# Performance work log

Hardware: AMD Instinct MI355X
Metric: run time of the kernel (lower is better)

The kernel has to match this reference:

```python
import jax, jax.numpy as jnp
import numpy as np

F = 256      # n_features
N = 128      # n_nodes
B = 4096     # batch


def setup_inputs() -> dict:
    key = jax.random.key(0)
    ks = jax.random.split(key, 11)
    s = lambda *sh: 1.0 / np.sqrt(sh[-2]) if len(sh) >= 2 else 1.0
    x = jax.random.normal(ks[0], (B, F), dtype=jnp.float32)
    # Block-diagonal weights: [F, in, out] per stage; biases [F, out]
    w1 = jax.random.normal(ks[1], (F, 1, N), dtype=jnp.float32)
    b1 = jax.random.normal(ks[2], (F, N), dtype=jnp.float32) * 0.01
    w2 = jax.random.normal(ks[3], (F, N, N), dtype=jnp.float32) / np.sqrt(N)
    b2 = jax.random.normal(ks[4], (F, N), dtype=jnp.float32) * 0.01
    w3 = jax.random.normal(ks[5], (F, N, N), dtype=jnp.float32) / np.sqrt(N)
    b3 = jax.random.normal(ks[6], (F, N), dtype=jnp.float32) * 0.01
    w4 = jax.random.normal(ks[7], (F, N, 1), dtype=jnp.float32) / np.sqrt(N)
    b4 = jax.random.normal(ks[8], (F, 1), dtype=jnp.float32) * 0.01
    # Final linear: [F, 1] weight, [1] bias
    lr_w = jax.random.normal(ks[9], (F, 1), dtype=jnp.float32) / np.sqrt(F)
    lr_b = jax.random.normal(ks[10], (1,), dtype=jnp.float32) * 0.01
    return {"x": x, "w1": w1, "b1": b1, "w2": w2, "b2": b2,
            "w3": w3, "b3": b3, "w4": w4, "b4": b4,
            "lr_w": lr_w, "lr_b": lr_b}


def reference(x, w1, b1, w2, b2, w3, b3, w4, b4, lr_w, lr_b):
    # Per-feature block-diagonal MLP chain with ReLU between stages.
    # x: [B, F] -> view each feature as a 1-dim input to its own subnet.
    h = x[:, :, None]                                   # [B, F, 1]
    h = jax.nn.relu(jnp.einsum('bfi,fio->bfo', h, w1) + b1)   # [B, F, N]
    h = jax.nn.relu(jnp.einsum('bfi,fio->bfo', h, w2) + b2)   # [B, F, N]
    h = jax.nn.relu(jnp.einsum('bfi,fio->bfo', h, w3) + b3)   # [B, F, N]
    h = jnp.einsum('bfi,fio->bfo', h, w4) + b4                # [B, F, 1]
    x_pre = h[:, :, 0]                                        # [B, F]
    return x_pre @ lr_w + lr_b                                # [B, 1]
```

## Files before the change

### kernel.cpp

```cpp
#include <hip/hip_runtime.h>
#include <hip/hip_bf16.h>

#define F_DIM 256
#define N_DIM 128
#define B_DIM 4096

typedef float f32x2v __attribute__((ext_vector_type(2)));
typedef float f32x4v __attribute__((ext_vector_type(4)));
typedef float f32x16v __attribute__((ext_vector_type(16)));
typedef short s16x8 __attribute__((ext_vector_type(8)));
typedef unsigned int u32x4v __attribute__((ext_vector_type(4)));

#define PIN(x) asm("" : "+v"(x))

__device__ __forceinline__ unsigned short f2bf(float f) {
  union { float f; unsigned u; } v; v.f = f;
  unsigned r = v.u + 0x7fffu + ((v.u >> 16) & 1u);
  return (unsigned short)(r >> 16);
}

__device__ __forceinline__ unsigned pk2(float a, float b) {
  union { __hip_bfloat16 h[2]; unsigned u; } v;
  v.h[0] = __float2bfloat16(a);
  v.h[1] = __float2bfloat16(b);
  return v.u;
}

__device__ __forceinline__ void gload16(const void* g, void* l) {
  __builtin_amdgcn_global_load_lds(
      (const __attribute__((address_space(1))) unsigned int*)g,
      (__attribute__((address_space(3))) unsigned int*)l, 16, 0, 0);
}

__device__ __forceinline__ s16x8 frag1(unsigned d) {
  u32x4v v = {d, 0u, 0u, 0u};
  return __builtin_bit_cast(s16x8, v);
}

struct frag2 { s16x8 lo, hi; };

__device__ __forceinline__ frag2 cvt2(f32x16v a) {
  unsigned P[8];
#pragma unroll
  for (int q = 0; q < 8; ++q) {
    unsigned pk = pk2(a[2 * q], a[2 * q + 1]);
    asm("v_pk_max_i16 %0, %1, 0" : "=v"(P[q]) : "v"(pk));
  }
  u32x4v lo = {P[0], P[1], P[2], P[3]};
  u32x4v hh = {P[4], P[5], P[6], P[7]};
  frag2 r;
  r.lo = __builtin_bit_cast(s16x8, lo);
  r.hi = __builtin_bit_cast(s16x8, hh);
  return r;
}

__global__ void prep_w(const float* __restrict__ w2, const float* __restrict__ w3,
                       unsigned int* __restrict__ wTs) {
  __shared__ float tile[128 * 130];
  int m = blockIdx.x;
  const float* src = (m < 256) ? (w2 + (size_t)m * 16384)
                               : (w3 + (size_t)(m - 256) * 16384);
  int t = threadIdx.x;
  for (int k = 0; k < 64; ++k) {
    int idx = k * 256 + t;
    int i = idx >> 7, o = idx & 127;
    tile[o * 130 + i] = src[idx];
  }
  __syncthreads();
  unsigned int* dst = wTs + (size_t)m * 8192;
  for (int k = 0; k < 32; ++k) {
    int idx = k * 256 + t;
    int o = idx >> 6, i2 = idx & 63;
    unsigned pk = (unsigned)f2bf(tile[o * 130 + 2 * i2]) |
                  ((unsigned)f2bf(tile[o * 130 + 2 * i2 + 1]) << 16);
    int w = i2 & 7;
    int i2p = (i2 & ~7) + ((w >> 1) & 1) * 4 + (w & 1) + (((w >> 2) & 1) << 1);
    dst[(o * 64) + (i2p ^ ((o & 15) << 2))] = pk;
  }
}

__global__ void prep_x(const float* __restrict__ x, float* __restrict__ xT) {
  __shared__ float tile[64][65];
  int btile = blockIdx.x & 63;
  int ftile = blockIdx.x >> 6;
  int t = threadIdx.x;
  for (int k = 0; k < 16; ++k) {
    int idx = k * 256 + t;
    int r = idx >> 6, c = idx & 63;
    tile[r][c] = x[(size_t)(btile * 64 + r) * F_DIM + ftile * 64 + c];
  }
  __syncthreads();
  for (int k = 0; k < 16; ++k) {
    int idx = k * 256 + t;
    int fr = idx >> 6, br = idx & 63;
    xT[(size_t)(ftile * 64 + fr) * B_DIM + btile * 64 + br] = tile[br][fr];
  }
}

__global__ __launch_bounds__(512, 2) void mlp_chain(
    const float* __restrict__ xT, const float* __restrict__ w1,
    const float* __restrict__ b1, const float* __restrict__ b2,
    const float* __restrict__ b3, const float* __restrict__ w4,
    const float* __restrict__ b4, const unsigned int* __restrict__ wTs,
    float* __restrict__ xp) {
  __shared__ __align__(16) char Wb[2][128 * 256];
  __shared__ __align__(16) float w4l[N_DIM];

  const int f    = blockIdx.x >> 1;
  const int half = blockIdx.x & 1;
  const int t    = threadIdx.x;
  const int lane = t & 63, wid = t >> 6;
  const int c32 = lane & 31, hi = lane >> 5;

  {
    const char* s2 = (const char*)(wTs + (size_t)f * 8192);
    const char* s3 = (const char*)(wTs + (size_t)(256 + f) * 8192);
#pragma unroll
    for (int c = 0; c < 4; ++c) {
      int off = (wid * 4 + c) * 1024;
      gload16(s2 + off + lane * 16, &Wb[0][off]);
    }
#pragma unroll
    for (int c = 0; c < 4; ++c) {
      int off = (wid * 4 + c) * 1024;
      gload16(s3 + off + lane * 16, &Wb[1][off]);
    }
    if (t < 32) *(f32x4v*)&w4l[t * 4] = *(const f32x4v*)&w4[f * N_DIM + t * 4];
  }

  unsigned a1d[4], a2d[4], a3d[4];
#pragma unroll
  for (int it = 0; it < 4; ++it) {
    int i = it * 32 + c32;
    float w1v = w1[f * N_DIM + i], b1v = b1[f * N_DIM + i];
    float b2v = b2[f * N_DIM + i], b3v = b3[f * N_DIM + i];
    a1d[it] = hi ? 0u : pk2(w1v, b1v);
    a2d[it] = hi ? 0u : pk2(0.f, b2v);
    a3d[it] = hi ? 0u : pk2(0.f, b3v);
  }
  const float b4f = b4[f];
  const float* xcol = xT + (size_t)f * B_DIM + half * 2048;
  float* xprow = xp + (size_t)f * B_DIM + half * 2048;

  const int wbase = c32 * 256 + (((lane & 15) ^ hi) << 4);
  int va[8];
#pragma unroll
  for (int m = 0; m < 8; ++m) { va[m] = wbase ^ (m << 5); PIN(va[m]); }
  const char* wb = &Wb[0][0];

  __syncthreads();

  const f32x16v zero = {0.f, 0.f, 0.f, 0.f, 0.f, 0.f, 0.f, 0.f,
                        0.f, 0.f, 0.f, 0.f, 0.f, 0.f, 0.f, 0.f};
  const f32x2v zz = {0.f, 0.f};

  float xvA = xcol[wid * 64 + c32];
  float xvB = xcol[wid * 64 + 32 + c32];
#pragma unroll 1
  for (int itb = 0; itb < 4; ++itb) {
    const int bb = itb * 512 + wid * 64;
    s16x8 BxA = frag1(hi ? 0u : pk2(xvA, 1.0f));
    s16x8 BxB = frag1(hi ? 0u : pk2(xvB, 1.0f));
    float xvA_n = (itb < 3) ? xcol[bb + 512 + c32] : 0.f;
    float xvB_n = (itb < 3) ? xcol[bb + 512 + 32 + c32] : 0.f;

    s16x8 h1A[8], h1B[8];
#pragma unroll
    for (int it = 0; it < 4; ++it) {
      f32x16v hA = __builtin_amdgcn_mfma_f32_32x32x16_bf16(frag1(a1d[it]), BxA,
                                                           zero, 0, 0, 0);
      frag2 rA = cvt2(hA);
      h1A[2 * it] = rA.lo;  h1A[2 * it + 1] = rA.hi;
      PIN(h1A[2 * it]);  PIN(h1A[2 * it + 1]);
      f32x16v hB = __builtin_amdgcn_mfma_f32_32x32x16_bf16(frag1(a1d[it]), BxB,
                                                           zero, 0, 0, 0);
      frag2 rB = cvt2(hB);
      h1B[2 * it] = rB.lo;  h1B[2 * it + 1] = rB.hi;
      PIN(h1B[2 * it]);  PIN(h1B[2 * it + 1]);
    }

    s16x8 h2A[8], h2B[8];
#pragma unroll
    for (int ntp = 0; ntp < 2; ++ntp) {
      const int nt0 = 2 * ntp, nt1 = nt0 + 1;
      f32x16v bi0 = __builtin_amdgcn_mfma_f32_32x32x16_bf16(frag1(a2d[nt0]), BxA,
                                                            zero, 0, 0, 0);
      f32x16v bi1 = __builtin_amdgcn_mfma_f32_32x32x16_bf16(frag1(a2d[nt1]), BxA,
                                                            zero, 0, 0, 0);
      f32x16v u0A, u0B, u1A, u1B;
      __builtin_amdgcn_s_setprio(1);
#pragma unroll
      for (int m = 0; m < 8; ++m) {
        s16x8 af0 = *(const s16x8*)(wb + va[m] + nt0 * 8192);
        s16x8 af1 = *(const s16x8*)(wb + va[m] + nt1 * 8192);
        u0A = __builtin_amdgcn_mfma_f32_32x32x16_bf16(af0, h1A[m],
                                                      m == 0 ? bi0 : u0A, 0, 0, 0);
        u0B = __builtin_amdgcn_mfma_f32_32x32x16_bf16(af0, h1B[m],
                                                      m == 0 ? bi0 : u0B, 0, 0, 0);
        u1A = __builtin_amdgcn_mfma_f32_32x32x16_bf16(af1, h1A[m],
                                                      m == 0 ? bi1 : u1A, 0, 0, 0);
        u1B = __builtin_amdgcn_mfma_f32_32x32x16_bf16(af1, h1B[m],
                                                      m == 0 ? bi1 : u1B, 0, 0, 0);
      }
      __builtin_amdgcn_s_setprio(0);
      frag2 r0A = cvt2(u0A);
      h2A[2 * nt0] = r0A.lo;  h2A[2 * nt0 + 1] = r0A.hi;
      PIN(h2A[2 * nt0]);  PIN(h2A[2 * nt0 + 1]);
      frag2 r0B = cvt2(u0B);
      h2B[2 * nt0] = r0B.lo;  h2B[2 * nt0 + 1] = r0B.hi;
      PIN(h2B[2 * nt0]);  PIN(h2B[2 * nt0 + 1]);
      frag2 r1A = cvt2(u1A);
      h2A[2 * nt1] = r1A.lo;  h2A[2 * nt1 + 1] = r1A.hi;
      PIN(h2A[2 * nt1]);  PIN(h2A[2 * nt1 + 1]);
      frag2 r1B = cvt2(u1B);
      h2B[2 * nt1] = r1B.lo;  h2B[2 * nt1 + 1] = r1B.hi;
      PIN(h2B[2 * nt1]);  PIN(h2B[2 * nt1 + 1]);
    }

    f32x2v pA0 = zz, pA1 = zz, pB0 = zz, pB1 = zz;
#pragma unroll
    for (int n3p = 0; n3p < 2; ++n3p) {
      const int n30 = 2 * n3p, n31 = n30 + 1;
      f32x16v ci0 = __builtin_amdgcn_mfma_f32_32x32x16_bf16(frag1(a3d[n30]), BxA,
                                                            zero, 0, 0, 0);
      f32x16v ci1 = __builtin_amdgcn_mfma_f32_32x32x16_bf16(frag1(a3d[n31]), BxA,
                                                            zero, 0, 0, 0);
      f32x16v v0A, v0B, v1A, v1B;
      __builtin_amdgcn_s_setprio(1);
#pragma unroll
      for (int k = 0; k < 8; ++k) {
        s16x8 af0 = *(const s16x8*)(wb + va[k] + 32768 + n30 * 8192);
        s16x8 af1 = *(const s16x8*)(wb + va[k] + 32768 + n31 * 8192);
        v0A = __builtin_amdgcn_mfma_f32_32x32x16_bf16(af0, h2A[k],
                                                      k == 0 ? ci0 : v0A, 0, 0, 0);
        v0B = __builtin_amdgcn_mfma_f32_32x32x16_bf16(af0, h2B[k],
                                                      k == 0 ? ci0 : v0B, 0, 0, 0);
        v1A = __builtin_amdgcn_mfma_f32_32x32x16_bf16(af1, h2A[k],
                                                      k == 0 ? ci1 : v1A, 0, 0, 0);
        v1B = __builtin_amdgcn_mfma_f32_32x32x16_bf16(af1, h2B[k],
                                                      k == 0 ? ci1 : v1B, 0, 0, 0);
      }
      __builtin_amdgcn_s_setprio(0);
#pragma unroll
      for (int q = 0; q < 4; ++q) {
        f32x2v w01_0 = *(const f32x2v*)&w4l[n30 * 32 + q * 8 + hi * 4];
        f32x2v w23_0 = *(const f32x2v*)&w4l[n30 * 32 + q * 8 + hi * 4 + 2];
        f32x2v w01_1 = *(const f32x2v*)&w4l[n31 * 32 + q * 8 + hi * 4];
        f32x2v w23_1 = *(const f32x2v*)&w4l[n31 * 32 + q * 8 + hi * 4 + 2];
        f32x2v r;
        r[0] = fmaxf(v0A[4 * q + 0], 0.f); r[1] = fmaxf(v0A[4 * q + 1], 0.f);
        pA0 += r * w01_0;
        r[0] = fmaxf(v0A[4 * q + 2], 0.f); r[1] = fmaxf(v0A[4 * q + 3], 0.f);
        pA1 += r * w23_0;
        r[0] = fmaxf(v1A[4 * q + 0], 0.f); r[1] = fmaxf(v1A[4 * q + 1], 0.f);
        pA0 += r * w01_1;
        r[0] = fmaxf(v1A[4 * q + 2], 0.f); r[1] = fmaxf(v1A[4 * q + 3], 0.f);
        pA1 += r * w23_1;
        r[0] = fmaxf(v0B[4 * q + 0], 0.f); r[1] = fmaxf(v0B[4 * q + 1], 0.f);
        pB0 += r * w01_0;
        r[0] = fmaxf(v0B[4 * q + 2], 0.f); r[1] = fmaxf(v0B[4 * q + 3], 0.f);
        pB1 += r * w23_0;
        r[0] = fmaxf(v1B[4 * q + 0], 0.f); r[1] = fmaxf(v1B[4 * q + 1], 0.f);
        pB0 += r * w01_1;
        r[0] = fmaxf(v1B[4 * q + 2], 0.f); r[1] = fmaxf(v1B[4 * q + 3], 0.f);
        pB1 += r * w23_1;
      }
    }
    float pA = pA0[0] + pA0[1] + pA1[0] + pA1[1];
    float pB = pB0[0] + pB0[1] + pB1[0] + pB1[1];
    pA += __shfl_xor(pA, 32, 64);
    pB += __shfl_xor(pB, 32, 64);
    if (hi == 0) {
      xprow[bb + c32]      = pA + b4f;
      xprow[bb + 32 + c32] = pB + b4f;
    }
    xvA = xvA_n;
    xvB = xvB_n;
  }
}

__global__ void final_reduce(const float* __restrict__ xp,
                             const float* __restrict__ lr_w,
                             const float* __restrict__ lr_b,
                             float* __restrict__ out) {
  __shared__ float lw[F_DIM];
  __shared__ float part[4][64];
  int t = threadIdx.x;
  if (t < F_DIM) lw[t] = lr_w[t];
  __syncthreads();
  int q = t >> 6, bl = t & 63;
  int b = blockIdx.x * 64 + bl;
  float acc = 0.f;
#pragma unroll 8
  for (int j = 0; j < 64; ++j) {
    int ff = q * 64 + j;
    acc += xp[(size_t)ff * B_DIM + b] * lw[ff];
  }
  part[q][bl] = acc;
  __syncthreads();
  if (q == 0)
    out[b] = part[0][bl] + part[1][bl] + part[2][bl] + part[3][bl] + lr_b[0];
}

extern "C" void kernel_launch(void* const* d_in, const int* in_sizes, int n_in,
                              void* d_out, int out_size, void* d_ws, size_t ws_size,
                              hipStream_t stream) {
  (void)in_sizes; (void)n_in; (void)out_size; (void)ws_size;
  const float* x    = (const float*)d_in[0];
  const float* w1   = (const float*)d_in[1];
  const float* b1   = (const float*)d_in[2];
  const float* w2   = (const float*)d_in[3];
  const float* b2   = (const float*)d_in[4];
  const float* w3   = (const float*)d_in[5];
  const float* b3   = (const float*)d_in[6];
  const float* w4   = (const float*)d_in[7];
  const float* b4   = (const float*)d_in[8];
  const float* lr_w = (const float*)d_in[9];
  const float* lr_b = (const float*)d_in[10];
  float* out = (float*)d_out;

  char* ws = (char*)d_ws;
  unsigned int* wTs = (unsigned int*)ws;
  float* xT = (float*)(ws + (16u << 20));
  float* xp = (float*)(ws + (16u << 20) + (4u << 20));

  prep_w<<<512, 256, 0, stream>>>(w2, w3, wTs);
  prep_x<<<256, 256, 0, stream>>>(x, xT);
  mlp_chain<<<512, 512, 0, stream>>>(xT, w1, b1, b2, b3, w4, b4, wTs, xp);
  final_reduce<<<64, 256, 0, stream>>>(xp, lr_w, lr_b, out);
}
```

Measured before the change: 92.73 us.

## Split each feature across four smaller blocks and prefetch LDS weight fragments

The MLP kernel now launches 1024 blocks of 256 threads, four per feature, in place of 512 blocks of 512 threads. This gives finer scheduling granularity but makes each block reload the full 64KB of w2/w3 weights into LDS. The stage-2 and stage-3 inner loops now load the first four weight fragments into registers before the bias MFMAs and fetch the second half while the first-half MFMAs run, to hide LDS latency. The extra fragment arrays raise register pressure, and the weight staging traffic from global memory doubles.

```diff
diff --git a/kernel.cpp b/kernel.cpp
--- a/kernel.cpp
+++ b/kernel.cpp
@@ -97,7 +97,7 @@
   }
 }
 
-__global__ __launch_bounds__(512, 2) void mlp_chain(
+__global__ __launch_bounds__(256, 2) void mlp_chain(
     const float* __restrict__ xT, const float* __restrict__ w1,
     const float* __restrict__ b1, const float* __restrict__ b2,
     const float* __restrict__ b3, const float* __restrict__ w4,
@@ -106,9 +106,9 @@
   __shared__ __align__(16) char Wb[2][128 * 256];
   __shared__ __align__(16) float w4l[N_DIM];
 
-  const int f    = blockIdx.x >> 1;
-  const int half = blockIdx.x & 1;
-  const int t    = threadIdx.x;
+  const int f  = blockIdx.x >> 2;
+  const int qt = blockIdx.x & 3;
+  const int t  = threadIdx.x;
   const int lane = t & 63, wid = t >> 6;
   const int c32 = lane & 31, hi = lane >> 5;
 
@@ -116,13 +116,13 @@
     const char* s2 = (const char*)(wTs + (size_t)f * 8192);
     const char* s3 = (const char*)(wTs + (size_t)(256 + f) * 8192);
 #pragma unroll
-    for (int c = 0; c < 4; ++c) {
-      int off = (wid * 4 + c) * 1024;
+    for (int c = 0; c < 8; ++c) {
+      int off = (wid * 8 + c) * 1024;
       gload16(s2 + off + lane * 16, &Wb[0][off]);
     }
 #pragma unroll
-    for (int c = 0; c < 4; ++c) {
-      int off = (wid * 4 + c) * 1024;
+    for (int c = 0; c < 8; ++c) {
+      int off = (wid * 8 + c) * 1024;
       gload16(s3 + off + lane * 16, &Wb[1][off]);
     }
     if (t < 32) *(f32x4v*)&w4l[t * 4] = *(const f32x4v*)&w4[f * N_DIM + t * 4];
@@ -139,8 +139,8 @@
     a3d[it] = hi ? 0u : pk2(0.f, b3v);
   }
   const float b4f = b4[f];
-  const float* xcol = xT + (size_t)f * B_DIM + half * 2048;
-  float* xprow = xp + (size_t)f * B_DIM + half * 2048;
+  const float* xcol = xT + (size_t)f * B_DIM + qt * 1024;
+  float* xprow = xp + (size_t)f * B_DIM + qt * 1024;
 
   const int wbase = c32 * 256 + (((lane & 15) ^ hi) << 4);
   int va[8];
@@ -158,11 +158,11 @@
   float xvB = xcol[wid * 64 + 32 + c32];
 #pragma unroll 1
   for (int itb = 0; itb < 4; ++itb) {
-    const int bb = itb * 512 + wid * 64;
+    const int bb = itb * 256 + wid * 64;
     s16x8 BxA = frag1(hi ? 0u : pk2(xvA, 1.0f));
     s16x8 BxB = frag1(hi ? 0u : pk2(xvB, 1.0f));
-    float xvA_n = (itb < 3) ? xcol[bb + 512 + c32] : 0.f;
-    float xvB_n = (itb < 3) ? xcol[bb + 512 + 32 + c32] : 0.f;
+    float xvA_n = (itb < 3) ? xcol[bb + 256 + c32] : 0.f;
+    float xvB_n = (itb < 3) ? xcol[bb + 256 + 32 + c32] : 0.f;
 
     s16x8 h1A[8], h1B[8];
 #pragma unroll
@@ -183,24 +183,40 @@
 #pragma unroll
     for (int ntp = 0; ntp < 2; ++ntp) {
       const int nt0 = 2 * ntp, nt1 = nt0 + 1;
+      s16x8 p0[4], p1[4];
+#pragma unroll
+      for (int j = 0; j < 4; ++j) {
+        p0[j] = *(const s16x8*)(wb + va[j] + nt0 * 8192);
+        p1[j] = *(const s16x8*)(wb + va[j] + nt1 * 8192);
+        PIN(p0[j]); PIN(p1[j]);
+      }
       f32x16v bi0 = __builtin_amdgcn_mfma_f32_32x32x16_bf16(frag1(a2d[nt0]), BxA,
                                                             zero, 0, 0, 0);
       f32x16v bi1 = __builtin_amdgcn_mfma_f32_32x32x16_bf16(frag1(a2d[nt1]), BxA,
                                                             zero, 0, 0, 0);
       f32x16v u0A, u0B, u1A, u1B;
+      s16x8 q0[4], q1[4];
       __builtin_amdgcn_s_setprio(1);
 #pragma unroll
-      for (int m = 0; m < 8; ++m) {
-        s16x8 af0 = *(const s16x8*)(wb + va[m] + nt0 * 8192);
-        s16x8 af1 = *(const s16x8*)(wb + va[m] + nt1 * 8192);
-        u0A = __builtin_amdgcn_mfma_f32_32x32x16_bf16(af0, h1A[m],
+      for (int m = 0; m < 4; ++m) {
+        q0[m] = *(const s16x8*)(wb + va[m + 4] + nt0 * 8192);
+        q1[m] = *(const s16x8*)(wb + va[m + 4] + nt1 * 8192);
+        PIN(q0[m]); PIN(q1[m]);
+        u0A = __builtin_amdgcn_mfma_f32_32x32x16_bf16(p0[m], h1A[m],
                                                       m == 0 ? bi0 : u0A, 0, 0, 0);
-        u0B = __builtin_amdgcn_mfma_f32_32x32x16_bf16(af0, h1B[m],
+        u0B = __builtin_amdgcn_mfma_f32_32x32x16_bf16(p0[m], h1B[m],
                                                       m == 0 ? bi0 : u0B, 0, 0, 0);
-        u1A = __builtin_amdgcn_mfma_f32_32x32x16_bf16(af1, h1A[m],
+        u1A = __builtin_amdgcn_mfma_f32_32x32x16_bf16(p1[m], h1A[m],
                                                       m == 0 ? bi1 : u1A, 0, 0, 0);
-        u1B = __builtin_amdgcn_mfma_f32_32x32x16_bf16(af1, h1B[m],
+        u1B = __builtin_amdgcn_mfma_f32_32x32x16_bf16(p1[m], h1B[m],
                                                       m == 0 ? bi1 : u1B, 0, 0, 0);
+      }
+#pragma unroll
+      for (int m = 0; m < 4; ++m) {
+        u0A = __builtin_amdgcn_mfma_f32_32x32x16_bf16(q0[m], h1A[m + 4], u0A, 0, 0, 0);
+        u0B = __builtin_amdgcn_mfma_f32_32x32x16_bf16(q0[m], h1B[m + 4], u0B, 0, 0, 0);
+        u1A = __builtin_amdgcn_mfma_f32_32x32x16_bf16(q1[m], h1A[m + 4], u1A, 0, 0, 0);
+        u1B = __builtin_amdgcn_mfma_f32_32x32x16_bf16(q1[m], h1B[m + 4], u1B, 0, 0, 0);
       }
       __builtin_amdgcn_s_setprio(0);
       frag2 r0A = cvt2(u0A);
@@ -221,24 +237,40 @@
 #pragma unroll
     for (int n3p = 0; n3p < 2; ++n3p) {
       const int n30 = 2 * n3p, n31 = n30 + 1;
+      s16x8 p0[4], p1[4];
+#pragma unroll
+      for (int j = 0; j < 4; ++j) {
+        p0[j] = *(const s16x8*)(wb + va[j] + 32768 + n30 * 8192);
+        p1[j] = *(const s16x8*)(wb + va[j] + 32768 + n31 * 8192);
+        PIN(p0[j]); PIN(p1[j]);
+      }
       f32x16v ci0 = __builtin_amdgcn_mfma_f32_32x32x16_bf16(frag1(a3d[n30]), BxA,
                                                             zero, 0, 0, 0);
       f32x16v ci1 = __builtin_amdgcn_mfma_f32_32x32x16_bf16(frag1(a3d[n31]), BxA,
                                                             zero, 0, 0, 0);
       f32x16v v0A, v0B, v1A, v1B;
+      s16x8 q0[4], q1[4];
       __builtin_amdgcn_s_setprio(1);
 #pragma unroll
-      for (int k = 0; k < 8; ++k) {
-        s16x8 af0 = *(const s16x8*)(wb + va[k] + 32768 + n30 * 8192);
-        s16x8 af1 = *(const s16x8*)(wb + va[k] + 32768 + n31 * 8192);
-        v0A = __builtin_amdgcn_mfma_f32_32x32x16_bf16(af0, h2A[k],
+      for (int k = 0; k < 4; ++k) {
+        q0[k] = *(const s16x8*)(wb + va[k + 4] + 32768 + n30 * 8192);
+        q1[k] = *(const s16x8*)(wb + va[k + 4] + 32768 + n31 * 8192);
+        PIN(q0[k]); PIN(q1[k]);
+        v0A = __builtin_amdgcn_mfma_f32_32x32x16_bf16(p0[k], h2A[k],
                                                       k == 0 ? ci0 : v0A, 0, 0, 0);
-        v0B = __builtin_amdgcn_mfma_f32_32x32x16_bf16(af0, h2B[k],
+        v0B = __builtin_amdgcn_mfma_f32_32x32x16_bf16(p0[k], h2B[k],
                                                       k == 0 ? ci0 : v0B, 0, 0, 0);
-        v1A = __builtin_amdgcn_mfma_f32_32x32x16_bf16(af1, h2A[k],
+        v1A = __builtin_amdgcn_mfma_f32_32x32x16_bf16(p1[k], h2A[k],
                                                       k == 0 ? ci1 : v1A, 0, 0, 0);
-        v1B = __builtin_amdgcn_mfma_f32_32x32x16_bf16(af1, h2B[k],
+        v1B = __builtin_amdgcn_mfma_f32_32x32x16_bf16(p1[k], h2B[k],
                                                       k == 0 ? ci1 : v1B, 0, 0, 0);
+      }
+#pragma unroll
+      for (int k = 0; k < 4; ++k) {
+        v0A = __builtin_amdgcn_mfma_f32_32x32x16_bf16(q0[k], h2A[k + 4], v0A, 0, 0, 0);
+        v0B = __builtin_amdgcn_mfma_f32_32x32x16_bf16(q0[k], h2B[k + 4], v0B, 0, 0, 0);
+        v1A = __builtin_amdgcn_mfma_f32_32x32x16_bf16(q1[k], h2A[k + 4], v1A, 0, 0, 0);
+        v1B = __builtin_amdgcn_mfma_f32_32x32x16_bf16(q1[k], h2B[k + 4], v1B, 0, 0, 0);
       }
       __builtin_amdgcn_s_setprio(0);
 #pragma unroll
@@ -326,6 +358,6 @@
 
   prep_w<<<512, 256, 0, stream>>>(w2, w3, wTs);
   prep_x<<<256, 256, 0, stream>>>(x, xT);
-  mlp_chain<<<512, 512, 0, stream>>>(xT, w1, b1, b2, b3, w4, b4, wTs, xp);
+  mlp_chain<<<1024, 256, 0, stream>>>(xT, w1, b1, b2, b3, w4, b4, wTs, xp);
   final_reduce<<<64, 256, 0, stream>>>(xp, lr_w, lr_b, out);
 }
```

Result: slower. 99.13 us (+6.9%).
